# Performance work log

Measured on AMD Instinct MI355X. Metric: run time of the kernel, lower is better.

## Reference

```python
import jax, jax.numpy as jnp
import numpy as np

P = 8          # patch_size = window_size // 3
C = 3          # in_channel (forced to 3 by the module's reshape logic)
QK_SCALE = 1.0


def _rel_bias(p):
    """Fixed relative-position bias [9, p, p], matching the torch constructor."""
    i = np.arange(p, dtype=np.float64)
    down = np.exp(-i / (p / 2))[:, None] * np.ones((1, p))   # down[i, :] = exp(-i/(p/2))
    right = down.T
    br = np.exp(-(i[:, None] + i[None, :]) / (p / 2))        # symmetric exp(-(i+j)/(p/2))
    merge = np.stack([
        np.rot90(br, 2), np.flip(down, 0), np.rot90(br, 1),
        np.flip(right, 1), np.ones((p, p)), right,
        np.rot90(br, 3), down, br,
    ], axis=0)
    return jnp.asarray(merge, dtype=jnp.float32)


def setup_inputs() -> dict:
    key = jax.random.key(0)
    k1, k2, k3 = jax.random.split(key, 3)
    b, c, h, w = 8, C, 512, 512
    d = c * P * P  # 192
    x = jax.random.normal(k1, (b, c, h, w), jnp.float32)
    W_qkv = jax.random.normal(k2, (3 * d, d), jnp.float32) * 0.05  # torch Linear weight [out, in]
    b_qkv = jax.random.normal(k3, (3 * d,), jnp.float32) * 0.01
    return {"x": x, "W_qkv": W_qkv, "b_qkv": b_qkv}


def reference(x, W_qkv, b_qkv):
    p, c = P, C
    b, _, h, w = x.shape
    nh, nw = h // p, w // p
    # pad by one patch on each side (zeros)
    xp = jnp.pad(x, ((0, 0), (0, 0), (p, p), (p, p)))
    # patch grid: [b, c, nh+2, p, nw+2, p] -> [b, nh+2, nw+2, c, p, p]
    g = xp.reshape(b, c, nh + 2, p, nw + 2, p).transpose(0, 2, 4, 1, 3, 5)
    # 9 neighbor patches per window, index k = 3*di + dj (row-major over 3x3 blocks)
    neigh = jnp.stack(
        [g[:, di:di + nh, dj:dj + nw] for di in range(3) for dj in range(3)],
        axis=3,
    )  # [b, nh, nw, 9, c, p, p]
    feat = neigh.reshape(b, nh, nw, 9, c * p * p)
    # qkv linear: y = feat @ W^T + b
    qkv = jnp.einsum('bijnd,ed->bijne', feat, W_qkv) + b_qkv  # [b, nh, nw, 9, 3*c*p*p]
    qkv = qkv.reshape(b, nh, nw, 9, 3, c, p, p)
    q = qkv[..., 0, :, :, :]  # [b, nh, nw, 9, c, p, p]
    k = qkv[..., 1, :, :, :]
    v = qkv[..., 2, :, :, :]
    core_q = q[:, :, :, 4] * QK_SCALE          # center patch query [b, nh, nw, c, p, p]
    bias = _rel_bias(p)                        # [9, p, p]
    # elementwise attention: (q * k * bias) * v, summed over the 9-neighbor window
    attn = core_q[:, :, :, None] * k * bias[:, None]   # [b, nh, nw, 9, c, p, p]
    out = jnp.sum(attn * v, axis=3)                    # [b, nh, nw, c, p, p]
    # reassemble to image: [b, c, nh, p, nw, p] -> [b, c, h, w]
    return out.transpose(0, 3, 1, 4, 2, 5).reshape(b, c, nh * p, nw * p)
```

## Files before the change

kernel.cpp:

```cpp
#include <hip/hip_runtime.h>


#define HW 512
#define PLANE 6291456

typedef __attribute__((ext_vector_type(8))) short bf16x8;
typedef __attribute__((ext_vector_type(4))) float f32x4;

static __device__ __forceinline__ unsigned short bf16_rne(float f) {
    unsigned u = __builtin_bit_cast(unsigned, f);
    u += 0x7FFFu + ((u >> 16) & 1u);
    return (unsigned short)(u >> 16);
}
static __device__ __forceinline__ float bf16f(unsigned short h) {
    unsigned u = ((unsigned)h) << 16;
    return __builtin_bit_cast(float, u);
}

__global__ void __launch_bounds__(256) wprep_kernel(const float* __restrict__ W,
                                                    unsigned short* __restrict__ Ws)
{
    int gid = blockIdx.x * 256 + threadIdx.x;
    int er  = gid % 192;
    int t   = gid / 192;
    int kg  = t & 7;
    int ckt = t >> 3;
    int c = ckt / 3, kt = ckt % 3;
    int slot = er >> 6, dl = er & 63;
    const float* src = W + (size_t)(slot*192 + c*64 + dl)*192 + kt*64 + kg*8;
    float4 a = ((const float4*)src)[0], b = ((const float4*)src)[1];
    float v[8] = {a.x, a.y, a.z, a.w, b.x, b.y, b.z, b.w};
    unsigned short h[8], lo[8];
    #pragma unroll
    for (int u = 0; u < 8; ++u) {
        h[u]  = bf16_rne(v[u]);
        lo[u] = bf16_rne(v[u] - bf16f(h[u]));
    }
    uint4 hp, lp;
    hp.x = (unsigned)h[0] | ((unsigned)h[1] << 16);
    hp.y = (unsigned)h[2] | ((unsigned)h[3] << 16);
    hp.z = (unsigned)h[4] | ((unsigned)h[5] << 16);
    hp.w = (unsigned)h[6] | ((unsigned)h[7] << 16);
    lp.x = (unsigned)lo[0] | ((unsigned)lo[1] << 16);
    lp.y = (unsigned)lo[2] | ((unsigned)lo[3] << 16);
    lp.z = (unsigned)lo[4] | ((unsigned)lo[5] << 16);
    lp.w = (unsigned)lo[6] | ((unsigned)lo[7] << 16);
    size_t oh = ((size_t)((ckt*2 + 0)*8 + kg)*192 + er) * 8;
    size_t ol = ((size_t)((ckt*2 + 1)*8 + kg)*192 + er) * 8;
    *(uint4*)(Ws + oh) = hp;
    *(uint4*)(Ws + ol) = lp;
}

__global__ void __launch_bounds__(256) qkv_mfma_kernel(
    const float* __restrict__ x,
    const unsigned short* __restrict__ Ws,
    const float* __restrict__ bqkv,
    float* __restrict__ ws)
{
    const int tid = threadIdx.x;
    const int mb  = blockIdx.x;
    const int c   = blockIdx.y;
    const int b   = mb >> 6, i = mb & 63;
    const int wv  = tid >> 6;
    const int l   = tid & 63;
    const int lr  = l & 15;
    const int lk  = l >> 4;

    f32x4 acc[4][3];
    #pragma unroll
    for (int m = 0; m < 4; ++m)
        #pragma unroll
        for (int n = 0; n < 3; ++n)
            #pragma unroll
            for (int r = 0; r < 4; ++r) acc[m][n][r] = 0.f;

    #pragma unroll
    for (int kt = 0; kt < 3; ++kt) {
        const float* xp = x + ((size_t)(b*3 + kt)*HW + (size_t)i*8) * HW;
        const unsigned short* Bb = Ws + (size_t)(c*3 + kt) * 2 * 8 * 192 * 8;
        #pragma unroll
        for (int ks = 0; ks < 2; ++ks) {
            const int pi = ks*4 + lk;
            bf16x8 ah[4], al[4];
            #pragma unroll
            for (int m = 0; m < 4; ++m) {
                int j = m*16 + lr;
                const float* ap = xp + (size_t)pi*HW + j*8;
                float4 a0 = *(const float4*)ap;
                float4 a1 = *(const float4*)(ap + 4);
                float v[8] = {a0.x, a0.y, a0.z, a0.w, a1.x, a1.y, a1.z, a1.w};
                #pragma unroll
                for (int u = 0; u < 8; ++u) {
                    unsigned short h = bf16_rne(v[u]);
                    ah[m][u] = (short)h;
                    al[m][u] = (short)bf16_rne(v[u] - bf16f(h));
                }
            }
            bf16x8 bh[3], bl[3];
            #pragma unroll
            for (int n = 0; n < 3; ++n) {
                int er = n*64 + wv*16 + lr;
                size_t oh = ((size_t)(0*8 + ks*4 + lk)*192 + er) * 8;
                size_t ol = ((size_t)(1*8 + ks*4 + lk)*192 + er) * 8;
                bh[n] = *(const bf16x8*)(Bb + oh);
                bl[n] = *(const bf16x8*)(Bb + ol);
            }
            #pragma unroll
            for (int m = 0; m < 4; ++m)
                #pragma unroll
                for (int n = 0; n < 3; ++n)
                    acc[m][n] = __builtin_amdgcn_mfma_f32_16x16x32_bf16(al[m], bh[n], acc[m][n], 0, 0, 0);
            #pragma unroll
            for (int m = 0; m < 4; ++m)
                #pragma unroll
                for (int n = 0; n < 3; ++n)
                    acc[m][n] = __builtin_amdgcn_mfma_f32_16x16x32_bf16(ah[m], bl[n], acc[m][n], 0, 0, 0);
            #pragma unroll
            for (int m = 0; m < 4; ++m)
                #pragma unroll
                for (int n = 0; n < 3; ++n)
                    acc[m][n] = __builtin_amdgcn_mfma_f32_16x16x32_bf16(ah[m], bh[n], acc[m][n], 0, 0, 0);
        }
    }

    const int dl = wv*16 + lr;
    const float bq = bqkv[      c*64 + dl];
    const float bk = bqkv[192 + c*64 + dl];
    const float bv = bqkv[384 + c*64 + dl];
    const int ppi = dl >> 3, ppj = dl & 7;
    float* qplane = ws;
    float* wplane = ws + PLANE;
    size_t rowoff = ((size_t)(b*3 + c)*HW + (size_t)(i*8 + ppi))*HW + ppj;
    #pragma unroll
    for (int m = 0; m < 4; ++m)
        #pragma unroll
        for (int ri = 0; ri < 4; ++ri) {
            int j = m*16 + lk*4 + ri;
            float qv  = acc[m][0][ri] + bq;
            float wvv = (acc[m][1][ri] + bk) * (acc[m][2][ri] + bv);
            qplane[rowoff + (size_t)j*8] = qv;
            wplane[rowoff + (size_t)j*8] = wvv;
        }
}

__global__ void __launch_bounds__(256) attn_kernel(
    const float* __restrict__ ws,
    const float* __restrict__ bqkv,
    float* __restrict__ out)
{
    __shared__ float wt[80][84];
    const int tid = threadIdx.x;
    int bid = blockIdx.x;
    int txt = (bid & 7) << 6;
    int tyt = ((bid >> 3) & 7) << 6;
    int pl  = bid >> 6;
    int c   = pl % 3;
    const float* qplane = ws + (size_t)pl * (HW*HW);
    const float* wplane = ws + PLANE + (size_t)pl * (HW*HW);

    const int pi  = (tid >> 4) & 7;
    const int pj0 = (tid & 1) << 2;
    const float fr0 = __expf((float)(pi - 7) * 0.25f);
    const float fr2 = __expf((float)(-pi) * 0.25f);
    float fa[4], fb[4];
    #pragma unroll
    for (int u = 0; u < 4; ++u) {
        int pj = pj0 + u;
        fa[u] = __expf((float)(pj - 7) * 0.25f);
        fb[u] = __expf((float)(-pj) * 0.25f);
    }

    for (int it = 0; it < 7; ++it) {
        int f = tid + it*256;
        if (f < 1600) {
            int r  = f / 20;
            int c4 = f - r*20;
            int gy = tyt - 8 + r;
            int gx = txt - 8 + (c4 << 2);
            float4 v;
            if ((unsigned)gy < 512u && (unsigned)gx < 512u) {
                v = *(const float4*)(wplane + (size_t)gy*HW + gx);
            } else {
                int d0 = c*64 + (gy & 7)*8 + (gx & 7);
                float4 bk = *(const float4*)(bqkv + 192 + d0);
                float4 bv = *(const float4*)(bqkv + 384 + d0);
                v.x = bk.x*bv.x; v.y = bk.y*bv.y; v.z = bk.z*bv.z; v.w = bk.w*bv.w;
            }
            *(float4*)&wt[r][c4 << 2] = v;
        }
    }
    __syncthreads();

    #pragma unroll
    for (int it = 0; it < 4; ++it) {
        int f  = tid + it*256;
        int ly = f >> 4;
        int lx = (f & 15) << 2;
        float sx = 0.f, sy = 0.f, sz = 0.f, sw = 0.f;
        #pragma unroll
        for (int di = 0; di < 3; ++di) {
            const float* row = &wt[ly + 8*di][lx];
            float4 w0 = *(const float4*)(row);
            float4 w1 = *(const float4*)(row + 8);
            float4 w2 = *(const float4*)(row + 16);
            float fr = (di == 0) ? fr0 : (di == 1) ? 1.f : fr2;
            sx += fr * (fa[0]*w0.x + w1.x + fb[0]*w2.x);
            sy += fr * (fa[1]*w0.y + w1.y + fb[1]*w2.y);
            sz += fr * (fa[2]*w0.z + w1.z + fb[2]*w2.z);
            sw += fr * (fa[3]*w0.w + w1.w + fb[3]*w2.w);
        }
        size_t off = (size_t)pl*(HW*HW) + (size_t)(tyt + ly)*HW + txt + lx;
        float4 q4 = *(const float4*)(qplane + (size_t)(tyt + ly)*HW + txt + lx);
        float4 o;
        o.x = q4.x*sx; o.y = q4.y*sy; o.z = q4.z*sz; o.w = q4.w*sw;
        *(float4*)(out + off) = o;
    }
}

extern "C" void kernel_launch(void* const* d_in, const int* in_sizes, int n_in,
                              void* d_out, int out_size, void* d_ws, size_t ws_size,
                              hipStream_t stream)
{
    const float* x  = (const float*)d_in[0];
    const float* W  = (const float*)d_in[1];
    const float* bq = (const float*)d_in[2];
    float* wsf = (float*)d_ws;
    unsigned short* Wsplit = (unsigned short*)(wsf + 2*(size_t)PLANE);

    wprep_kernel<<<54, 256, 0, stream>>>(W, Wsplit);
    qkv_mfma_kernel<<<dim3(512, 3), 256, 0, stream>>>(x, Wsplit, bq, wsf);
    attn_kernel<<<1536, 256, 0, stream>>>(wsf, bq, (float*)d_out);
}
```

Before: 122.5 us.

## Store intermediate q and k*v planes in fp16 and split x by truncation

The q plane and the k*v product plane in the workspace are stored as fp16 instead of fp32, which halves the traffic of the intermediate write and the attention kernel's reads. The attention tile loader now fetches 8 halves per thread and converts them to float. Separately, splitting x into bf16 hi/lo parts uses bit truncation with byte permutes instead of round-to-nearest, cutting ALU work in the GEMM. The risks are fp16 range and precision loss on the intermediates and a slightly less accurate hi/lo split.

```diff
diff --git a/kernel.cpp b/kernel.cpp
--- a/kernel.cpp
+++ b/kernel.cpp
@@ -1,4 +1,5 @@
 #include <hip/hip_runtime.h>
+#include <hip/hip_fp16.h>
 
 
 #define HW 512
@@ -6,6 +7,7 @@
 
 typedef __attribute__((ext_vector_type(8))) short bf16x8;
 typedef __attribute__((ext_vector_type(4))) float f32x4;
+typedef __attribute__((ext_vector_type(4))) unsigned int u32x4;
 
 static __device__ __forceinline__ unsigned short bf16_rne(float f) {
     unsigned u = __builtin_bit_cast(unsigned, f);
@@ -15,6 +17,12 @@
 static __device__ __forceinline__ float bf16f(unsigned short h) {
     unsigned u = ((unsigned)h) << 16;
     return __builtin_bit_cast(float, u);
+}
+static __device__ __forceinline__ float ubits_f(unsigned u) {
+    return __builtin_bit_cast(float, u);
+}
+static __device__ __forceinline__ unsigned f_ubits(float f) {
+    return __builtin_bit_cast(unsigned, f);
 }
 
 __global__ void __launch_bounds__(256) wprep_kernel(const float* __restrict__ W,
@@ -55,7 +63,7 @@
     const float* __restrict__ x,
     const unsigned short* __restrict__ Ws,
     const float* __restrict__ bqkv,
-    float* __restrict__ ws)
+    __half* __restrict__ ws)
 {
     const int tid = threadIdx.x;
     const int mb  = blockIdx.x;
@@ -86,15 +94,28 @@
             for (int m = 0; m < 4; ++m) {
                 int j = m*16 + lr;
                 const float* ap = xp + (size_t)pi*HW + j*8;
-                float4 a0 = *(const float4*)ap;
-                float4 a1 = *(const float4*)(ap + 4);
-                float v[8] = {a0.x, a0.y, a0.z, a0.w, a1.x, a1.y, a1.z, a1.w};
-                #pragma unroll
-                for (int u = 0; u < 8; ++u) {
-                    unsigned short h = bf16_rne(v[u]);
-                    ah[m][u] = (short)h;
-                    al[m][u] = (short)bf16_rne(v[u] - bf16f(h));
-                }
+                uint4 a0 = *(const uint4*)ap;
+                uint4 a1 = *(const uint4*)(ap + 4);
+                unsigned h01 = __builtin_amdgcn_perm(a0.y, a0.x, 0x07060302u);
+                unsigned h23 = __builtin_amdgcn_perm(a0.w, a0.z, 0x07060302u);
+                unsigned h45 = __builtin_amdgcn_perm(a1.y, a1.x, 0x07060302u);
+                unsigned h67 = __builtin_amdgcn_perm(a1.w, a1.z, 0x07060302u);
+                unsigned l0 = f_ubits(ubits_f(a0.x) - ubits_f(a0.x & 0xFFFF0000u));
+                unsigned l1 = f_ubits(ubits_f(a0.y) - ubits_f(a0.y & 0xFFFF0000u));
+                unsigned l2 = f_ubits(ubits_f(a0.z) - ubits_f(a0.z & 0xFFFF0000u));
+                unsigned l3 = f_ubits(ubits_f(a0.w) - ubits_f(a0.w & 0xFFFF0000u));
+                unsigned l4 = f_ubits(ubits_f(a1.x) - ubits_f(a1.x & 0xFFFF0000u));
+                unsigned l5 = f_ubits(ubits_f(a1.y) - ubits_f(a1.y & 0xFFFF0000u));
+                unsigned l6 = f_ubits(ubits_f(a1.z) - ubits_f(a1.z & 0xFFFF0000u));
+                unsigned l7 = f_ubits(ubits_f(a1.w) - ubits_f(a1.w & 0xFFFF0000u));
+                unsigned q01 = __builtin_amdgcn_perm(l1, l0, 0x07060302u);
+                unsigned q23 = __builtin_amdgcn_perm(l3, l2, 0x07060302u);
+                unsigned q45 = __builtin_amdgcn_perm(l5, l4, 0x07060302u);
+                unsigned q67 = __builtin_amdgcn_perm(l7, l6, 0x07060302u);
+                u32x4 hv = {h01, h23, h45, h67};
+                u32x4 lv = {q01, q23, q45, q67};
+                ah[m] = __builtin_bit_cast(bf16x8, hv);
+                al[m] = __builtin_bit_cast(bf16x8, lv);
             }
             bf16x8 bh[3], bl[3];
             #pragma unroll
@@ -128,8 +149,8 @@
     const float bk = bqkv[192 + c*64 + dl];
     const float bv = bqkv[384 + c*64 + dl];
     const int ppi = dl >> 3, ppj = dl & 7;
-    float* qplane = ws;
-    float* wplane = ws + PLANE;
+    __half* qplane = ws;
+    __half* wplane = ws + PLANE;
     size_t rowoff = ((size_t)(b*3 + c)*HW + (size_t)(i*8 + ppi))*HW + ppj;
     #pragma unroll
     for (int m = 0; m < 4; ++m)
@@ -138,13 +159,13 @@
             int j = m*16 + lk*4 + ri;
             float qv  = acc[m][0][ri] + bq;
             float wvv = (acc[m][1][ri] + bk) * (acc[m][2][ri] + bv);
-            qplane[rowoff + (size_t)j*8] = qv;
-            wplane[rowoff + (size_t)j*8] = wvv;
+            qplane[rowoff + (size_t)j*8] = __float2half_rn(qv);
+            wplane[rowoff + (size_t)j*8] = __float2half_rn(wvv);
         }
 }
 
 __global__ void __launch_bounds__(256) attn_kernel(
-    const float* __restrict__ ws,
+    const __half* __restrict__ ws,
     const float* __restrict__ bqkv,
     float* __restrict__ out)
 {
@@ -155,8 +176,8 @@
     int tyt = ((bid >> 3) & 7) << 6;
     int pl  = bid >> 6;
     int c   = pl % 3;
-    const float* qplane = ws + (size_t)pl * (HW*HW);
-    const float* wplane = ws + PLANE + (size_t)pl * (HW*HW);
+    const __half* qplane = ws + (size_t)pl * (HW*HW);
+    const __half* wplane = ws + PLANE + (size_t)pl * (HW*HW);
 
     const int pi  = (tid >> 4) & 7;
     const int pj0 = (tid & 1) << 2;
@@ -170,23 +191,35 @@
         fb[u] = __expf((float)(-pj) * 0.25f);
     }
 
-    for (int it = 0; it < 7; ++it) {
+    #pragma unroll
+    for (int it = 0; it < 4; ++it) {
         int f = tid + it*256;
-        if (f < 1600) {
-            int r  = f / 20;
-            int c4 = f - r*20;
+        if (f < 800) {
+            int r  = f / 10;
+            int c8 = f - r*10;
             int gy = tyt - 8 + r;
-            int gx = txt - 8 + (c4 << 2);
-            float4 v;
+            int gx = txt - 8 + c8*8;
+            float o[8];
             if ((unsigned)gy < 512u && (unsigned)gx < 512u) {
-                v = *(const float4*)(wplane + (size_t)gy*HW + gx);
+                uint4 hv = *(const uint4*)(wplane + (size_t)gy*HW + gx);
+                const __half2* hp = (const __half2*)&hv;
+                #pragma unroll
+                for (int t = 0; t < 4; ++t) {
+                    float2 f2 = __half22float2(hp[t]);
+                    o[2*t] = f2.x; o[2*t+1] = f2.y;
+                }
             } else {
-                int d0 = c*64 + (gy & 7)*8 + (gx & 7);
-                float4 bk = *(const float4*)(bqkv + 192 + d0);
-                float4 bv = *(const float4*)(bqkv + 384 + d0);
-                v.x = bk.x*bv.x; v.y = bk.y*bv.y; v.z = bk.z*bv.z; v.w = bk.w*bv.w;
+                int d0 = c*64 + (gy & 7)*8;
+                float4 k0 = *(const float4*)(bqkv + 192 + d0);
+                float4 k1 = *(const float4*)(bqkv + 196 + d0);
+                float4 v0 = *(const float4*)(bqkv + 384 + d0);
+                float4 v1 = *(const float4*)(bqkv + 388 + d0);
+                o[0]=k0.x*v0.x; o[1]=k0.y*v0.y; o[2]=k0.z*v0.z; o[3]=k0.w*v0.w;
+                o[4]=k1.x*v1.x; o[5]=k1.y*v1.y; o[6]=k1.z*v1.z; o[7]=k1.w*v1.w;
             }
-            *(float4*)&wt[r][c4 << 2] = v;
+            float* dst = &wt[r][c8*8];
+            *(float4*)dst       = make_float4(o[0], o[1], o[2], o[3]);
+            *(float4*)(dst + 4) = make_float4(o[4], o[5], o[6], o[7]);
         }
     }
     __syncthreads();
@@ -209,10 +242,12 @@
             sz += fr * (fa[2]*w0.z + w1.z + fb[2]*w2.z);
             sw += fr * (fa[3]*w0.w + w1.w + fb[3]*w2.w);
         }
+        const __half* qp = qplane + (size_t)(tyt + ly)*HW + txt + lx;
+        float2 q01 = __half22float2(*(const __half2*)qp);
+        float2 q23 = __half22float2(*(const __half2*)(qp + 2));
         size_t off = (size_t)pl*(HW*HW) + (size_t)(tyt + ly)*HW + txt + lx;
-        float4 q4 = *(const float4*)(qplane + (size_t)(tyt + ly)*HW + txt + lx);
         float4 o;
-        o.x = q4.x*sx; o.y = q4.y*sy; o.z = q4.z*sz; o.w = q4.w*sw;
+        o.x = q01.x*sx; o.y = q01.y*sy; o.z = q23.x*sz; o.w = q23.y*sw;
         *(float4*)(out + off) = o;
     }
 }
@@ -224,10 +259,10 @@
     const float* x  = (const float*)d_in[0];
     const float* W  = (const float*)d_in[1];
     const float* bq = (const float*)d_in[2];
-    float* wsf = (float*)d_ws;
-    unsigned short* Wsplit = (unsigned short*)(wsf + 2*(size_t)PLANE);
+    __half* wsh = (__half*)d_ws;
+    unsigned short* Wsplit = (unsigned short*)(wsh + 2*(size_t)PLANE);
 
     wprep_kernel<<<54, 256, 0, stream>>>(W, Wsplit);
-    qkv_mfma_kernel<<<dim3(512, 3), 256, 0, stream>>>(x, Wsplit, bq, wsf);
-    attn_kernel<<<1536, 256, 0, stream>>>(wsf, bq, (float*)d_out);
-}
+    qkv_mfma_kernel<<<dim3(512, 3), 256, 0, stream>>>(x, Wsplit, bq, wsh);
+    attn_kernel<<<1536, 256, 0, stream>>>(wsh, bq, (float*)d_out);
+}
```

Result: faster. 115.7 us (-5.5%).
